# Kernel tuning notes

Hardware: AMD Instinct MI355X
Metric: run time of the kernel (lower is better)

## Reference

```python
import jax, jax.numpy as jnp
from jax import lax
import numpy as np

B, L, D_MODEL = 2, 2048, 1024
D_INNER, D_STATE, D_CONV, DT_RANK = 2048, 16, 4, 64


def setup_inputs() -> dict:
    key = jax.random.key(0)
    ks = jax.random.split(key, 10)
    s = 0.02  # weight scale to keep activations numerically sane
    return {
        "x": jax.random.normal(ks[0], (B, L, D_MODEL), jnp.float32),
        "W_in": jax.random.normal(ks[1], (D_MODEL, 2 * D_INNER), jnp.float32) * s,
        "conv_w": jax.random.normal(ks[2], (D_INNER, D_CONV), jnp.float32) * 0.2,
        "conv_b": jax.random.normal(ks[3], (D_INNER,), jnp.float32) * 0.1,
        "W_xproj": jax.random.normal(ks[4], (D_INNER, DT_RANK + 2 * D_STATE), jnp.float32) * s,
        "W_dt": jax.random.normal(ks[5], (DT_RANK, D_INNER), jnp.float32) * (DT_RANK ** -0.5),
        "b_dt": jax.random.normal(ks[6], (D_INNER,), jnp.float32) * 0.1,
        "A_log": jax.random.uniform(ks[7], (D_INNER, D_STATE), jnp.float32),
        "D_skip": jnp.ones((D_INNER,), jnp.float32),
        "W_out": jax.random.normal(ks[8], (D_INNER, D_MODEL), jnp.float32) * s,
    }


def _causal_depthwise_conv(xt, w, b):
    # xt: (B, L, d_inner), w: (d_inner, d_conv). Torch pads both sides by d_conv-1
    # then slices [:L] => causal left-pad of d_conv-1.
    xc = jnp.moveaxis(xt, 1, 2)  # (B, d_inner, L)
    out = lax.conv_general_dilated(
        xc, w[:, None, :], window_strides=(1,),
        padding=[(D_CONV - 1, 0)], feature_group_count=D_INNER)
    return jnp.moveaxis(out, 1, 2) + b  # (B, L, d_inner)


def _selective_scan(u, delta, A, Bm, Cm, D_skip):
    # u, delta: (B, L, d_inner); A: (d_inner, d_state); Bm, Cm: (B, L, d_state)
    deltaA = jnp.exp(delta[..., None] * A)                  # (B,L,di,ds)
    dBu = (delta * u)[..., None] * Bm[:, :, None, :]        # (B,L,di,ds)

    def step(h, inp):
        dA_t, dBu_t, C_t = inp                              # (B,di,ds),(B,di,ds),(B,ds)
        h = dA_t * h + dBu_t
        y = jnp.einsum('bds,bs->bd', h, C_t)
        return h, y

    h0 = jnp.zeros((u.shape[0], D_INNER, D_STATE), u.dtype)
    xs = (jnp.moveaxis(deltaA, 1, 0), jnp.moveaxis(dBu, 1, 0), jnp.moveaxis(Cm, 1, 0))
    _, ys = lax.scan(step, h0, xs)                          # ys: (L,B,di)
    return jnp.moveaxis(ys, 0, 1) + u * D_skip


def reference(x, W_in, conv_w, conv_b, W_xproj, W_dt, b_dt, A_log, D_skip, W_out):
    xz = x @ W_in                                           # (B,L,2*di)
    xin, z = jnp.split(xz, 2, axis=-1)
    xc = jax.nn.silu(_causal_depthwise_conv(xin, conv_w, conv_b))
    dbc = xc @ W_xproj                                      # (B,L,dt_rank+2*ds)
    dt_lo = dbc[..., :DT_RANK]
    Bm = dbc[..., DT_RANK:DT_RANK + D_STATE]
    Cm = dbc[..., DT_RANK + D_STATE:]
    delta = jax.nn.softplus(dt_lo @ W_dt + b_dt)            # (B,L,di)
    A = -jnp.exp(A_log)
    y = _selective_scan(xc, delta, A, Bm, Cm, D_skip)
    return (y * jax.nn.silu(z)) @ W_out                     # (B,L,d_model)
```

## Files before the change

kernel.cpp:

```cpp
#include <hip/hip_runtime.h>
#include <math.h>

#define B_SZ 2
#define L_SZ 2048
#define DMODEL 1024
#define DINNER 2048
#define DSTATE 16
#define DCONV 4
#define DTRANK 64

#define CS 32
#define NCH (L_SZ / CS)

typedef float f32x4 __attribute__((ext_vector_type(4)));
typedef __bf16 bf16x8 __attribute__((ext_vector_type(8)));

__device__ __forceinline__ float silu_f(float x) {
    return x / (1.0f + __expf(-x));
}

__device__ __forceinline__ float softplus_f(float x) {
    return fmaxf(x, 0.0f) + __logf(1.0f + __expf(-fabsf(x)));
}

__device__ __forceinline__ unsigned short f2bf(float x) {
    unsigned int u = __float_as_uint(x);
    u = u + 0x7FFFu + ((u >> 16) & 1u);
    return (unsigned short)(u >> 16);
}

__device__ __forceinline__ float bf2f(unsigned short s) {
    return __uint_as_float(((unsigned int)s) << 16);
}

__device__ __forceinline__ void gload_lds16(const unsigned short* g, unsigned short* l) {
    __builtin_amdgcn_global_load_lds(
        (const __attribute__((address_space(1))) void*)g,
        (__attribute__((address_space(3))) void*)l, 16, 0, 0);
}

union Pack8 { unsigned short s[8]; uint4 v; };

__global__ __launch_bounds__(256) void transpose_cast(
    const float* __restrict__ W, unsigned short* __restrict__ WT, int R, int C)
{
    __shared__ float t[32][33];
    const int tx = threadIdx.x & 31;
    const int ty = threadIdx.x >> 5;
    const int r0 = blockIdx.y * 32;
    const int c0 = blockIdx.x * 32;
    #pragma unroll
    for (int i = 0; i < 4; i++)
        t[ty + i * 8][tx] = W[(r0 + ty + i * 8) * C + c0 + tx];
    __syncthreads();
    #pragma unroll
    for (int i = 0; i < 4; i++)
        WT[(c0 + ty + i * 8) * R + r0 + tx] = f2bf(t[tx][ty + i * 8]);
}

__global__ __launch_bounds__(256) void cast_bf16(
    const float* __restrict__ src, unsigned short* __restrict__ dst, int n8)
{
    int i = blockIdx.x * 256 + threadIdx.x;
    if (i >= n8) return;
    const float4 f0 = *(const float4*)(src + i * 8);
    const float4 f1 = *(const float4*)(src + i * 8 + 4);
    Pack8 p;
    p.s[0] = f2bf(f0.x); p.s[1] = f2bf(f0.y); p.s[2] = f2bf(f0.z); p.s[3] = f2bf(f0.w);
    p.s[4] = f2bf(f1.x); p.s[5] = f2bf(f1.y); p.s[6] = f2bf(f1.z); p.s[7] = f2bf(f1.w);
    *(uint4*)(dst + i * 8) = p.v;
}

template <int ACT, int OBF16>
__global__ __launch_bounds__(256) void gemm_bt_lds(
    const unsigned short* __restrict__ A, const unsigned short* __restrict__ BT,
    void* __restrict__ Cout, const float* __restrict__ bias,
    int M, int N, int K, int lda, int ldb, int ldc, int Kc)
{
    __shared__ unsigned short As[128 * 64];
    __shared__ unsigned short Bs[128 * 64];

    const int tid  = threadIdx.x;
    const int lane = tid & 63;
    const int wave = tid >> 6;
    const int wm   = wave >> 1;
    const int wn   = wave & 1;
    const int row0 = blockIdx.y * 128;
    const int col0 = blockIdx.x * 128;
    const int lq   = lane >> 4;
    const int lm   = lane & 15;
    const int kbeg = blockIdx.z * Kc;

    const int rloc = wave * 32 + (lane >> 3);
    const int sc   = (lane & 7) ^ ((lane >> 3) & 7);
    const unsigned short* gA = A + (size_t)(row0 + rloc) * lda + sc * 8;
    const unsigned short* gBp[4];
    #pragma unroll
    for (int is = 0; is < 4; is++) {
        int br = col0 + rloc + 8 * is;
        if (br > N - 1) br = N - 1;
        gBp[is] = BT + (size_t)br * ldb + sc * 8;
    }
    unsigned short* lA = As + wave * 2048;
    unsigned short* lB = Bs + wave * 2048;

    f32x4 acc[4][4];
    #pragma unroll
    for (int i = 0; i < 4; i++)
        #pragma unroll
        for (int j = 0; j < 4; j++)
            #pragma unroll
            for (int r = 0; r < 4; r++) acc[i][j][r] = 0.0f;

    for (int k0 = kbeg; k0 < kbeg + Kc; k0 += 64) {
        #pragma unroll
        for (int is = 0; is < 4; is++) {
            gload_lds16(gA + (size_t)(8 * is) * lda + k0, lA + is * 512);
            gload_lds16(gBp[is] + k0, lB + is * 512);
        }
        __syncthreads();

        #pragma unroll
        for (int ks = 0; ks < 2; ks++) {
            bf16x8 af[4], bfr[4];
            #pragma unroll
            for (int i = 0; i < 4; i++) {
                int row = wm * 64 + i * 16 + lm;
                af[i] = *(const bf16x8*)&As[row * 64 + (((ks * 4 + lq) ^ (row & 7)) * 8)];
            }
            #pragma unroll
            for (int j = 0; j < 4; j++) {
                int row = wn * 64 + j * 16 + lm;
                bfr[j] = *(const bf16x8*)&Bs[row * 64 + (((ks * 4 + lq) ^ (row & 7)) * 8)];
            }
            #pragma unroll
            for (int i = 0; i < 4; i++)
                #pragma unroll
                for (int j = 0; j < 4; j++)
                    acc[i][j] = __builtin_amdgcn_mfma_f32_16x16x32_bf16(
                        af[i], bfr[j], acc[i][j], 0, 0, 0);
        }
        __syncthreads();
    }

    #pragma unroll
    for (int i = 0; i < 4; i++) {
        #pragma unroll
        for (int r = 0; r < 4; r++) {
            int row = row0 + wm * 64 + i * 16 + lq * 4 + r;
            #pragma unroll
            for (int j = 0; j < 4; j++) {
                int col = col0 + wn * 64 + j * 16 + lm;
                if (col < N) {
                    float v = acc[i][j][r];
                    if (ACT == 1) v = softplus_f(v + bias[col]);
                    if (OBF16) {
                        unsigned short* Cz = (unsigned short*)Cout +
                            (size_t)blockIdx.z * (size_t)M * ldc;
                        Cz[(size_t)row * ldc + col] = f2bf(v);
                    } else {
                        float* Cz = (float*)Cout +
                            (size_t)blockIdx.z * (size_t)M * ldc;
                        Cz[(size_t)row * ldc + col] = v;
                    }
                }
            }
        }
    }
}

__global__ __launch_bounds__(256) void reduce_splitk(
    const float* __restrict__ part, float* __restrict__ C,
    unsigned short* __restrict__ dtlo16, int n, int nsplit)
{
    int i = blockIdx.x * 256 + threadIdx.x;
    if (i >= n) return;
    float s = 0.0f;
    for (int z = 0; z < nsplit; z++) s += part[(size_t)z * n + i];
    C[i] = s;
    int row = i / 96;
    int col = i - row * 96;
    if (col < DTRANK) dtlo16[row * DTRANK + col] = f2bf(s);
}

__global__ __launch_bounds__(256) void conv_silu_v2(
    const unsigned short* __restrict__ xz16, const float* __restrict__ conv_w,
    const float* __restrict__ conv_b, unsigned short* __restrict__ xc16)
{
    const int tid = threadIdx.x;
    const int d   = blockIdx.x * 256 + tid;
    const int l0  = blockIdx.y * 32;
    const int b   = blockIdx.z;
    const float4 w  = *(const float4*)(conv_w + d * 4);
    const float bias = conv_b[d];
    const int t0 = b * L_SZ + l0;
    const unsigned short* src = xz16 + (size_t)t0 * 4096 + d;

    float r0, r1, r2;
    if (l0 == 0) {
        r0 = r1 = r2 = 0.0f;
    } else {
        r0 = bf2f(src[-3 * 4096]);
        r1 = bf2f(src[-2 * 4096]);
        r2 = bf2f(src[-1 * 4096]);
    }
    #pragma unroll 4
    for (int l = 0; l < 32; l++) {
        float r3 = bf2f(src[(size_t)l * 4096]);
        float acc = bias + r0 * w.x + r1 * w.y + r2 * w.z + r3 * w.w;
        xc16[(size_t)(t0 + l) * DINNER + d] = f2bf(silu_f(acc));
        r0 = r1; r1 = r2; r2 = r3;
    }
}

__global__ __launch_bounds__(256) void scan_pass1(
    const unsigned short* __restrict__ xc16, const float* __restrict__ delta,
    const float* __restrict__ dbc, const float* __restrict__ A_log,
    float* __restrict__ P, float* __restrict__ E)
{
    __shared__ float Bs[CS * DSTATE];
    const int tid = threadIdx.x;
    const int db  = blockIdx.x & 7;
    const int c   = (blockIdx.x >> 3) & (NCH - 1);
    const int b   = blockIdx.x >> 9;
    const int d   = db * 256 + tid;
    const int t0  = b * L_SZ + c * CS;

    for (int idx = tid; idx < CS * DSTATE; idx += 256) {
        int step = idx >> 4, i = idx & 15;
        Bs[idx] = dbc[(t0 + step) * 96 + DTRANK + i];
    }

    float A[DSTATE], Er[DSTATE];
    #pragma unroll
    for (int s = 0; s < DSTATE; s++) {
        A[s]  = -__expf(A_log[d * DSTATE + s]);
        Er[s] = 0.0f;
    }
    float sd = 0.0f;
    __syncthreads();

    for (int l = 0; l < CS; l++) {
        const int t = t0 + l;
        float dv = delta[t * DINNER + d];
        float uv = bf2f(xc16[(size_t)t * DINNER + d]);
        float du = dv * uv;
        sd += dv;
        #pragma unroll
        for (int s = 0; s < DSTATE; s++) {
            float dA = __expf(dv * A[s]);
            Er[s] = dA * Er[s] + du * Bs[l * DSTATE + s];
        }
    }

    const long long o = ((long long)((b * NCH + c) * DINNER) + d) * DSTATE;
    #pragma unroll
    for (int s = 0; s < DSTATE; s++) {
        P[o + s] = __expf(A[s] * sd);
        E[o + s] = Er[s];
    }
}

__global__ __launch_bounds__(256) void scan_pass2(
    const float* __restrict__ P, float* __restrict__ E)
{
    const int gid  = blockIdx.x * 256 + threadIdx.x;
    const int b    = gid >> 15;
    const int rest = gid & 32767;
    float h = 0.0f;
    for (int c = 0; c < NCH; c++) {
        const long long idx = (long long)(b * NCH + c) * (DINNER * DSTATE) + rest;
        float p = P[idx];
        float e = E[idx];
        E[idx] = h;
        h = p * h + e;
    }
}

__global__ __launch_bounds__(256) void scan_pass3(
    const unsigned short* __restrict__ xc16, const float* __restrict__ delta,
    const float* __restrict__ dbc, const float* __restrict__ A_log,
    const float* __restrict__ D_skip, const float* __restrict__ Hin,
    const unsigned short* __restrict__ xz16, unsigned short* __restrict__ y16)
{
    __shared__ float BCs[CS * 2 * DSTATE];
    const int tid = threadIdx.x;
    const int db  = blockIdx.x & 7;
    const int c   = (blockIdx.x >> 3) & (NCH - 1);
    const int b   = blockIdx.x >> 9;
    const int d   = db * 256 + tid;
    const int t0  = b * L_SZ + c * CS;

    for (int idx = tid; idx < CS * 2 * DSTATE; idx += 256) {
        int step = idx >> 5, i = idx & 31;
        BCs[idx] = dbc[(t0 + step) * 96 + DTRANK + i];
    }

    float A[DSTATE], h[DSTATE];
    const long long o = ((long long)((b * NCH + c) * DINNER) + d) * DSTATE;
    #pragma unroll
    for (int s = 0; s < DSTATE; s++) {
        A[s] = -__expf(A_log[d * DSTATE + s]);
        h[s] = Hin[o + s];
    }
    const float Dv = D_skip[d];
    __syncthreads();

    for (int l = 0; l < CS; l++) {
        const int t = t0 + l;
        float dv = delta[t * DINNER + d];
        float uv = bf2f(xc16[(size_t)t * DINNER + d]);
        float du = dv * uv;
        float yv = 0.0f;
        #pragma unroll
        for (int s = 0; s < DSTATE; s++) {
            float dA = __expf(dv * A[s]);
            h[s] = dA * h[s] + du * BCs[l * 32 + s];
            yv  += h[s] * BCs[l * 32 + DSTATE + s];
        }
        float z = bf2f(xz16[(size_t)t * 4096 + DINNER + d]);
        y16[t * DINNER + d] = f2bf((uv * Dv + yv) * silu_f(z));
    }
}

extern "C" void kernel_launch(void* const* d_in, const int* in_sizes, int n_in,
                              void* d_out, int out_size, void* d_ws, size_t ws_size,
                              hipStream_t stream) {
    const float* x       = (const float*)d_in[0];
    const float* W_in    = (const float*)d_in[1];
    const float* conv_w  = (const float*)d_in[2];
    const float* conv_b  = (const float*)d_in[3];
    const float* W_xproj = (const float*)d_in[4];
    const float* W_dt    = (const float*)d_in[5];
    const float* b_dt    = (const float*)d_in[6];
    const float* A_log   = (const float*)d_in[7];
    const float* D_skip  = (const float*)d_in[8];
    const float* W_out   = (const float*)d_in[9];
    float* out = (float*)d_out;

    float* ws = (float*)d_ws;
    unsigned short* xz16   = (unsigned short*)ws;
    unsigned short* xc16   = (unsigned short*)(ws +  8388608);
    float* dbc             = ws + 12582912;
    unsigned short* dtlo16 = (unsigned short*)(ws + 12976128);
    float* delta           = ws + 13107200;
    float* Ebuf            = ws + 21495808;
    float* Pbuf            = ws + 25690112;
    float* parts           = Pbuf;
    unsigned short* yb16   = (unsigned short*)(ws + 29884416);
    unsigned short* x16    = yb16;
    unsigned short* W_inT    = (unsigned short*)(ws + 31981568);
    unsigned short* W_xprojT = (unsigned short*)(ws + 34078720);
    unsigned short* W_dtT    = (unsigned short*)(ws + 34177024);
    unsigned short* W_outT   = (unsigned short*)(ws + 34242560);

    const int MT = 4096;

    transpose_cast<<<dim3(128, 32), 256, 0, stream>>>(W_in,    W_inT,    1024, 4096);
    transpose_cast<<<dim3(  3, 64), 256, 0, stream>>>(W_xproj, W_xprojT, 2048,   96);
    transpose_cast<<<dim3( 64,  2), 256, 0, stream>>>(W_dt,    W_dtT,      64, 2048);
    transpose_cast<<<dim3( 32, 64), 256, 0, stream>>>(W_out,   W_outT,   2048, 1024);
    cast_bf16<<<dim3(2048), 256, 0, stream>>>(x, x16, 524288);

    gemm_bt_lds<0, 1><<<dim3(32, 32), 256, 0, stream>>>(
        x16, W_inT, xz16, nullptr, MT, 4096, 1024, 1024, 1024, 4096, 1024);

    conv_silu_v2<<<dim3(8, 64, 2), 256, 0, stream>>>(xz16, conv_w, conv_b, xc16);

    gemm_bt_lds<0, 0><<<dim3(1, 32, 8), 256, 0, stream>>>(
        xc16, W_xprojT, parts, nullptr, MT, 96, 2048, 2048, 2048, 96, 256);
    reduce_splitk<<<dim3(1536), 256, 0, stream>>>(parts, dbc, dtlo16, MT * 96, 8);

    gemm_bt_lds<1, 0><<<dim3(16, 32), 256, 0, stream>>>(
        dtlo16, W_dtT, delta, b_dt, MT, 2048, 64, 64, 64, 2048, 64);

    scan_pass1<<<dim3(1024), 256, 0, stream>>>(xc16, delta, dbc, A_log, Pbuf, Ebuf);
    scan_pass2<<<dim3(256), 256, 0, stream>>>(Pbuf, Ebuf);
    scan_pass3<<<dim3(1024), 256, 0, stream>>>(xc16, delta, dbc, A_log, D_skip,
                                               Ebuf, xz16, yb16);

    gemm_bt_lds<0, 0><<<dim3(8, 32), 256, 0, stream>>>(
        yb16, W_outT, out, nullptr, MT, 1024, 2048, 2048, 2048, 1024, 2048);
}
```

Before: 326.9 us.

## Use 256x256-tile double-buffered MFMA GEMM for the input projection

Adds a new GEMM kernel with 256x256 output tiles, 512 threads, XOR-swizzled LDS, direct global-to-LDS loads double-buffered across K, and an XCD-aware block remap. It replaces the in-projection GEMM (4096x4096x1024). Larger tiles raise operand reuse and cut global traffic, and overlapping the loads is meant to hide memory latency. In exchange the kernel needs 128KB of LDS and many accumulator registers, and the grid has only 256 blocks.

```diff
diff --git a/kernel.cpp b/kernel.cpp
--- a/kernel.cpp
+++ b/kernel.cpp
@@ -169,6 +169,122 @@
     }
 }
 
+template <int OBF16>
+__global__ __launch_bounds__(512, 2) void gemm_bt_256(
+    const unsigned short* __restrict__ A, const unsigned short* __restrict__ BT,
+    void* __restrict__ Cout, int M, int N, int K, int lda, int ldb, int ldc)
+{
+    __shared__ unsigned short sm[2][2][256 * 64];
+
+    const int tid  = threadIdx.x;
+    const int lane = tid & 63;
+    const int wave = tid >> 6;
+    const int wm   = wave >> 2;
+    const int wn   = wave & 3;
+    const int lq   = lane >> 4;
+    const int lm   = lane & 15;
+
+    const int cpx = gridDim.x >> 3;
+    const int ti  = (blockIdx.x & 7) * cpx + (blockIdx.x >> 3);
+    const int nbx = N >> 8;
+    const int bx  = ti % nbx;
+    const int by  = ti / nbx;
+    const int row0 = by * 256;
+    const int col0 = bx * 256;
+
+    const int rA = tid >> 3;
+    const int sc = (tid & 7) ^ (rA & 7);
+    const unsigned short* gA = A + (size_t)(row0 + rA) * lda + sc * 8;
+    const unsigned short* gB[4];
+    #pragma unroll
+    for (int a = 0; a < 4; a++) {
+        int br = col0 + a * 64 + rA;
+        if (br > N - 1) br = N - 1;
+        gB[a] = BT + (size_t)br * ldb + sc * 8;
+    }
+
+    auto STAGE = [&](int bsel, int kk) {
+        #pragma unroll
+        for (int a = 0; a < 4; a++) {
+            gload_lds16(gA + (size_t)(a * 64) * lda + kk,
+                        &sm[bsel][0][a * 4096 + wave * 512]);
+            gload_lds16(gB[a] + kk,
+                        &sm[bsel][1][a * 4096 + wave * 512]);
+        }
+    };
+
+    f32x4 acc[8][4];
+    #pragma unroll
+    for (int i = 0; i < 8; i++)
+        #pragma unroll
+        for (int j = 0; j < 4; j++)
+            #pragma unroll
+            for (int r = 0; r < 4; r++) acc[i][j][r] = 0.0f;
+
+    const int NT = K >> 6;
+    STAGE(0, 0);
+    STAGE(1, 64);
+
+    for (int t = 0; t < NT; ++t) {
+        if (t < NT - 1) {
+            asm volatile("s_waitcnt vmcnt(8)" ::: "memory");
+        } else {
+            asm volatile("s_waitcnt vmcnt(0)" ::: "memory");
+        }
+        __builtin_amdgcn_s_barrier();
+        __builtin_amdgcn_sched_barrier(0);
+
+        const int b = t & 1;
+        #pragma unroll
+        for (int ks = 0; ks < 2; ks++) {
+            bf16x8 af[8], bq[4];
+            #pragma unroll
+            for (int i = 0; i < 8; i++) {
+                int row = wm * 128 + i * 16 + lm;
+                af[i] = *(const bf16x8*)&sm[b][0][row * 64 +
+                            (((ks * 4 + lq) ^ (row & 7)) * 8)];
+            }
+            #pragma unroll
+            for (int j = 0; j < 4; j++) {
+                int row = wn * 64 + j * 16 + lm;
+                bq[j] = *(const bf16x8*)&sm[b][1][row * 64 +
+                            (((ks * 4 + lq) ^ (row & 7)) * 8)];
+            }
+            #pragma unroll
+            for (int i = 0; i < 8; i++)
+                #pragma unroll
+                for (int j = 0; j < 4; j++)
+                    acc[i][j] = __builtin_amdgcn_mfma_f32_16x16x32_bf16(
+                        af[i], bq[j], acc[i][j], 0, 0, 0);
+        }
+
+        asm volatile("s_waitcnt lgkmcnt(0)" ::: "memory");
+        __builtin_amdgcn_sched_barrier(0);
+        __builtin_amdgcn_s_barrier();
+        __builtin_amdgcn_sched_barrier(0);
+        if (t + 2 < NT) STAGE(b, (t + 2) * 64);
+    }
+
+    #pragma unroll
+    for (int i = 0; i < 8; i++) {
+        #pragma unroll
+        for (int r = 0; r < 4; r++) {
+            int row = row0 + wm * 128 + i * 16 + lq * 4 + r;
+            #pragma unroll
+            for (int j = 0; j < 4; j++) {
+                int col = col0 + wn * 64 + j * 16 + lm;
+                if (col < N) {
+                    float v = acc[i][j][r];
+                    if (OBF16)
+                        ((unsigned short*)Cout)[(size_t)row * ldc + col] = f2bf(v);
+                    else
+                        ((float*)Cout)[(size_t)row * ldc + col] = v;
+                }
+            }
+        }
+    }
+}
+
 __global__ __launch_bounds__(256) void reduce_splitk(
     const float* __restrict__ part, float* __restrict__ C,
     unsigned short* __restrict__ dtlo16, int n, int nsplit)
@@ -362,8 +478,8 @@
     transpose_cast<<<dim3( 32, 64), 256, 0, stream>>>(W_out,   W_outT,   2048, 1024);
     cast_bf16<<<dim3(2048), 256, 0, stream>>>(x, x16, 524288);
 
-    gemm_bt_lds<0, 1><<<dim3(32, 32), 256, 0, stream>>>(
-        x16, W_inT, xz16, nullptr, MT, 4096, 1024, 1024, 1024, 4096, 1024);
+    gemm_bt_256<1><<<dim3(256), 512, 0, stream>>>(
+        x16, W_inT, xz16, MT, 4096, 1024, 1024, 1024, 4096);
 
     conv_silu_v2<<<dim3(8, 64, 2), 256, 0, stream>>>(xz16, conv_w, conv_b, xc16);
 
```

New measurement: 319.3 us. -2.3%, faster.
